# Optimization experiments

Measured on AMD Instinct MI355X. Metric: run time of the kernel, lower is better.

## Reference

```python
import jax, jax.numpy as jnp
import numpy as np

N_POINTS = 524288
N_VOXELS = 32768
C_IN = 6
GF = 64          # gf_dim
C_OUT = 256      # output_channels
HALF = C_OUT // 2


def _linear_params(key, fin, fout):
    kw, kb = jax.random.split(key)
    bound = 1.0 / np.sqrt(fin)
    W = jax.random.uniform(kw, (fin, fout), jnp.float32, -bound, bound)
    b = jax.random.uniform(kb, (fout,), jnp.float32, -bound, bound)
    return W, b


def setup_inputs() -> dict:
    key = jax.random.key(0)
    ks = jax.random.split(key, 8)
    inp_feat = jax.random.normal(ks[0], (N_POINTS, C_IN), dtype=jnp.float32)
    vox2point_idx = jax.random.randint(ks[1], (N_POINTS,), 0, N_VOXELS, dtype=jnp.int64)
    W1, b1 = _linear_params(ks[2], C_IN, GF)          # point_lin1
    W2, b2 = _linear_params(ks[3], GF, HALF)          # point_lin2
    Wv1, bv1 = _linear_params(ks[4], HALF, HALF)      # vox_lin1
    W3, b3 = _linear_params(ks[5], C_OUT, C_OUT)      # point_lin3
    W4, b4 = _linear_params(ks[6], C_OUT, C_OUT)      # point_lin4
    Wv2, bv2 = _linear_params(ks[7], C_OUT, C_OUT)    # vox_lin2
    return {
        "inp_feat": inp_feat, "vox2point_idx": vox2point_idx, "num_voxels": N_VOXELS,
        "W1": W1, "b1": b1, "W2": W2, "b2": b2, "Wv1": Wv1, "bv1": bv1,
        "W3": W3, "b3": b3, "W4": W4, "b4": b4, "Wv2": Wv2, "bv2": bv2,
    }


def reference(inp_feat, vox2point_idx, num_voxels,
              W1, b1, W2, b2, Wv1, bv1, W3, b3, W4, b4, Wv2, bv2):
    relu = jax.nn.relu
    # per-point MLP: [N,6] -> [N,64] -> [N,128]
    point_feat1 = relu(inp_feat @ W1 + b1)
    point_feat2 = relu(point_feat1 @ W2 + b2)
    # scatter-max pooling over voxels: [N,128] -> [V,128]
    occ_voxel_feat = jax.ops.segment_max(point_feat2, vox2point_idx,
                                         num_segments=num_voxels)
    occ_voxel_feat = relu(occ_voxel_feat @ Wv1 + bv1)
    # gather voxel feature back to points and concat: [N,128]+[N,128] -> [N,256]
    point_global_feat = occ_voxel_feat[vox2point_idx]
    point_feat3 = jnp.concatenate((point_global_feat, point_feat2), axis=-1)
    point_feat4 = relu(point_feat3 @ W3 + b3)
    point_feat5 = relu(point_feat4 @ W4 + b4)
    # second scatter-max pooling: [N,256] -> [V,256]
    occ_voxel_feat2 = jax.ops.segment_max(point_feat5, vox2point_idx,
                                          num_segments=num_voxels)
    occ_voxel_feat2 = relu(occ_voxel_feat2 @ Wv2 + bv2)
    return occ_voxel_feat2
```

## Files before the change

### kernel.cpp

```cpp
#include <hip/hip_runtime.h>


#define NPTS 524288
#define NVOX 32768

typedef _Float16 f16;
typedef _Float16 f16x8 __attribute__((ext_vector_type(8)));
typedef float f32x4 __attribute__((ext_vector_type(4)));

#define GLDS16(g, l)                                                          \
  __builtin_amdgcn_global_load_lds(                                           \
      (const __attribute__((address_space(1))) unsigned int*)(const void*)(g),\
      (__attribute__((address_space(3))) unsigned int*)(void*)(l), 16, 0, 0)

__global__ void k_fixidx(const int* __restrict__ raw, int* __restrict__ out) {
  bool is64 = true;
#pragma unroll
  for (int k = 0; k < 32; ++k)
    if (raw[2 * k + 1] != 0) is64 = false;
  int stride = gridDim.x * blockDim.x;
  for (int i = blockIdx.x * blockDim.x + threadIdx.x; i < NPTS; i += stride)
    out[i] = is64 ? raw[2 * i] : raw[i];
}

__global__ void k_hist(const int* __restrict__ idx, int* __restrict__ counts) {
  int stride = gridDim.x * blockDim.x;
  for (int i = blockIdx.x * blockDim.x + threadIdx.x; i < NPTS; i += stride)
    atomicAdd(&counts[idx[i]], 1);
}

__global__ void k_scan(const int* __restrict__ counts, int* __restrict__ offsets) {
  __shared__ int part[1024];
  __shared__ int sums[32];
  int t = threadIdx.x;
  int loc[32];
  int s = 0;
#pragma unroll
  for (int j = 0; j < 32; ++j) { loc[j] = counts[t * 32 + j]; s += loc[j]; }
  part[t] = s;
  __syncthreads();
  if (t < 32) {
    int run = 0;
    for (int j = 0; j < 32; ++j) { int tmp = part[t * 32 + j]; part[t * 32 + j] = run; run += tmp; }
    sums[t] = run;
  }
  __syncthreads();
  if (t == 0) {
    int run = 0;
    for (int i = 0; i < 32; ++i) { int tmp = sums[i]; sums[i] = run; run += tmp; }
  }
  __syncthreads();
  int b = part[t] + sums[t >> 5];
#pragma unroll
  for (int j = 0; j < 32; ++j) { offsets[t * 32 + j] = b; b += loc[j]; }
  if (t == 1023) offsets[NVOX] = b;
}

__global__ void k_scat(const int* __restrict__ idx, const int* __restrict__ offsets,
                       int* __restrict__ cursor, int* __restrict__ sp, int* __restrict__ sv) {
  int stride = gridDim.x * blockDim.x;
  for (int i = blockIdx.x * blockDim.x + threadIdx.x; i < NPTS; i += stride) {
    int v = idx[i];
    int pos = offsets[v] + atomicAdd(&cursor[v], 1);
    sp[pos] = i;
    sv[pos] = v;
  }
}

__global__ void k_wcast(const float* __restrict__ W, f16* __restrict__ Wt, int K, int N) {
  int g = blockIdx.x * blockDim.x + threadIdx.x;
  if (g >= K * N) return;
  int k = g / N, n = g % N;
  Wt[n * K + k] = (f16)W[g];
}

__global__ void k_castf(const float* __restrict__ in, f16* __restrict__ out, int n) {
  int stride = gridDim.x * blockDim.x;
  for (int i = blockIdx.x * blockDim.x + threadIdx.x; i < n; i += stride)
    out[i] = (f16)in[i];
}

template <int K, int N, int MODEA, bool SCATTER, bool OUTF32, bool WRITEO>
__global__ __launch_bounds__(256, 3) void k_gemm(
    const f16* __restrict__ A,
    const int* __restrict__ sv, const int* __restrict__ sp,
    const int* __restrict__ offs,
    const float* __restrict__ x, const float* __restrict__ W1, const float* __restrict__ b1,
    const f16* __restrict__ Bt,
    const float* __restrict__ bias,
    f16* __restrict__ Of16, float* __restrict__ Of32, int row0) {
  constexpr int NT = N / 128;
  __shared__ __align__(16) char smem[32768];
  __shared__ float xs[MODEA == 2 ? 768 : 1];
  __shared__ int svp[MODEA == 2 ? 128 : 1];
  __shared__ int svx[SCATTER ? 128 : 1];
  f16* As = (f16*)smem;
  f16* Bs = As + 128 * 64;

  int nwg = gridDim.x;
  int bid = blockIdx.x;
  int q = nwg >> 3;
  int swz = (bid & 7) * q + (bid >> 3);
  int tm = swz / NT, tn = swz % NT;
  int t = threadIdx.x;

  if (MODEA == 2) { if (t < 128) svp[t] = sp[row0 + tm * 128 + t]; }
  if (SCATTER) { if (t < 128) svx[t] = sv[row0 + tm * 128 + t]; }
  if (MODEA == 2) __syncthreads();

  int l = t & 63, w = t >> 6;
  int wm = w >> 1, wn = w & 1;
  int lrow = l & 15, lk = l >> 4;
  f32x4 acc[4][4] = {};

  constexpr int KT = K / 64;
#pragma unroll
  for (int kt = 0; kt < KT; ++kt) {
    int k0 = kt * 64;
#pragma unroll
    for (int i = 0; i < 4; ++i) {
      int n = i * 32 + (t >> 3);
      int clog = (t & 7) ^ (n & 7);
      GLDS16(Bt + (size_t)(tn * 128 + n) * K + k0 + clog * 8, Bs + i * 2048 + t * 8);
    }
    if constexpr (MODEA == 2) {
      for (int g = t; g < 768; g += 256) xs[g] = x[(size_t)svp[g / 6] * 6 + (g % 6)];
      __syncthreads();
      int j = t & 63;
      float wv[6];
#pragma unroll
      for (int i = 0; i < 6; ++i) wv[i] = W1[i * 64 + j];
      float bb = b1[j];
      int rb = (t >> 6) * 32;
#pragma unroll
      for (int rr = 0; rr < 32; ++rr) {
        int row = rb + rr;
        float a = bb;
#pragma unroll
        for (int i = 0; i < 6; ++i) a += xs[row * 6 + i] * wv[i];
        As[row * 64 + (((j >> 3) ^ (row & 7)) << 3) + (j & 7)] = (f16)fmaxf(a, 0.f);
      }
    } else {
#pragma unroll
      for (int i = 0; i < 4; ++i) {
        int row = i * 32 + (t >> 3);
        int clog = (t & 7) ^ (row & 7);
        GLDS16(A + (size_t)(tm * 128 + row) * K + k0 + clog * 8, As + i * 2048 + t * 8);
      }
    }
    __syncthreads();
#pragma unroll
    for (int ks = 0; ks < 2; ++ks) {
      f16x8 af[4], bf[4];
#pragma unroll
      for (int m = 0; m < 4; ++m) {
        int row = wm * 64 + m * 16 + lrow;
        int cp = (ks * 4 + lk) ^ (row & 7);
        af[m] = *(const f16x8*)(As + row * 64 + cp * 8);
      }
#pragma unroll
      for (int n = 0; n < 4; ++n) {
        int col = wn * 64 + n * 16 + lrow;
        int cp = (ks * 4 + lk) ^ (col & 7);
        bf[n] = *(const f16x8*)(Bs + col * 64 + cp * 8);
      }
#pragma unroll
      for (int m = 0; m < 4; ++m)
#pragma unroll
        for (int n = 0; n < 4; ++n)
          acc[m][n] = __builtin_amdgcn_mfma_f32_16x16x32_f16(af[m], bf[n], acc[m][n], 0, 0, 0);
    }
    __syncthreads();
  }

  if constexpr (WRITEO) {
#pragma unroll
    for (int m = 0; m < 4; ++m)
#pragma unroll
      for (int n = 0; n < 4; ++n)
#pragma unroll
        for (int j = 0; j < 4; ++j) {
          int row = wm * 64 + m * 16 + lk * 4 + j;
          int gc  = tn * 128 + wn * 64 + n * 16 + lrow;
          float val = fmaxf(acc[m][n][j] + bias[gc], 0.f);
          if constexpr (OUTF32) Of32[(size_t)(tm * 128 + row) * N + gc] = val;
          else                  Of16[(size_t)(tm * 128 + row) * N + gc] = (f16)val;
        }
  }

  if constexpr (SCATTER) {
    f16* tile = (f16*)smem;
#pragma unroll
    for (int m = 0; m < 4; ++m)
#pragma unroll
      for (int n = 0; n < 4; ++n)
#pragma unroll
        for (int j = 0; j < 4; ++j) {
          int row = wm * 64 + m * 16 + lk * 4 + j;
          int col = wn * 64 + n * 16 + lrow;
          tile[row * 128 + col] =
              (f16)fmaxf(acc[m][n][j] + bias[tn * 128 + col], 0.f);
        }
    __syncthreads();
    int c = t & 127, h = t >> 7;
    int r0l = h * 64;
    int gc = tn * 128 + c;
    int grow0 = row0 + tm * 128 + r0l;
    float run = 0.f;
    int curv = svx[r0l];
    for (int r = r0l; r < r0l + 64; ++r) {
      int v = svx[r];
      if (v != curv) {
        bool inter = (offs[curv] >= grow0) && (offs[curv + 1] <= grow0 + 64);
        if (inter) Of32[(size_t)curv * N + gc] = run;
        else atomicMax((int*)&Of32[(size_t)curv * N + gc], __float_as_int(run));
        curv = v; run = 0.f;
      }
      run = fmaxf(run, (float)tile[r * 128 + c]);
    }
    bool inter = (offs[curv] >= grow0) && (offs[curv + 1] <= grow0 + 64);
    if (inter) Of32[(size_t)curv * N + gc] = run;
    else atomicMax((int*)&Of32[(size_t)curv * N + gc], __float_as_int(run));
  }
}

__global__ __launch_bounds__(512, 2) void k_stage2(
    const f16* __restrict__ pf2, const f16* __restrict__ occ1,
    const int* __restrict__ sv, const int* __restrict__ offs,
    const f16* __restrict__ W3t, const float* __restrict__ b3,
    const f16* __restrict__ W4t, const float* __restrict__ b4,
    float* __restrict__ vox2f, int row0) {
  __shared__ __align__(16) char smem[8192 + 33792 + 33792];
  __shared__ int svx[64];
  f16* As  = (f16*)smem;
  f16* Bs  = (f16*)(smem + 8192);
  f16* pf5 = Bs;
  f16* pf4 = (f16*)(smem + 8192 + 33792);

  int nwg = gridDim.x;
  int bid = blockIdx.x;
  int q = nwg >> 3;
  int bm = (bid & 7) * q + (bid >> 3);
  int t = threadIdx.x;
  if (t < 64) svx[t] = sv[row0 + bm * 64 + t];
  __syncthreads();

  int l = t & 63, w = t >> 6;
  int lrow = l & 15, lk = l >> 4;

  {
    f32x4 acc[4][2] = {};
#pragma unroll
    for (int kt = 0; kt < 4; ++kt) {
      int k0 = kt * 64;
#pragma unroll
      for (int i = 0; i < 4; ++i) {
        int g = i * 512 + t;
        int n = g >> 3;
        int clog = (g & 7) ^ (n & 7);
        GLDS16(W3t + (size_t)n * 256 + k0 + clog * 8, Bs + g * 8);
      }
      {
        int r = t >> 3;
        int clog = (t & 7) ^ (r & 7);
        const f16* src;
        if (k0 < 128) src = occ1 + (size_t)svx[r] * 128 + k0 + clog * 8;
        else          src = pf2 + (size_t)(bm * 64 + r) * 128 + (k0 - 128) + clog * 8;
        GLDS16(src, As + t * 8);
      }
      __syncthreads();
#pragma unroll
      for (int ks = 0; ks < 2; ++ks) {
        f16x8 af[4], bf[2];
#pragma unroll
        for (int m = 0; m < 4; ++m) {
          int row = m * 16 + lrow;
          int cp = (ks * 4 + lk) ^ (row & 7);
          af[m] = *(const f16x8*)(As + row * 64 + cp * 8);
        }
#pragma unroll
        for (int n = 0; n < 2; ++n) {
          int col = w * 32 + n * 16 + lrow;
          int cp = (ks * 4 + lk) ^ (col & 7);
          bf[n] = *(const f16x8*)(Bs + col * 64 + cp * 8);
        }
#pragma unroll
        for (int m = 0; m < 4; ++m)
#pragma unroll
          for (int n = 0; n < 2; ++n)
            acc[m][n] = __builtin_amdgcn_mfma_f32_16x16x32_f16(af[m], bf[n], acc[m][n], 0, 0, 0);
      }
      __syncthreads();
    }
#pragma unroll
    for (int m = 0; m < 4; ++m)
#pragma unroll
      for (int n = 0; n < 2; ++n)
#pragma unroll
        for (int j = 0; j < 4; ++j) {
          int row  = m * 16 + lk * 4 + j;
          int colg = w * 32 + n * 16 + lrow;
          pf4[row * 264 + colg] = (f16)fmaxf(acc[m][n][j] + b3[colg], 0.f);
        }
  }
  __syncthreads();

  {
    f32x4 acc[4][2] = {};
#pragma unroll
    for (int kt = 0; kt < 4; ++kt) {
      int k0 = kt * 64;
#pragma unroll
      for (int i = 0; i < 4; ++i) {
        int g = i * 512 + t;
        int n = g >> 3;
        int clog = (g & 7) ^ (n & 7);
        GLDS16(W4t + (size_t)n * 256 + k0 + clog * 8, Bs + g * 8);
      }
      __syncthreads();
#pragma unroll
      for (int ks = 0; ks < 2; ++ks) {
        f16x8 af[4], bf[2];
#pragma unroll
        for (int m = 0; m < 4; ++m) {
          int row = m * 16 + lrow;
          int chunk = kt * 8 + ks * 4 + lk;
          af[m] = *(const f16x8*)(pf4 + row * 264 + chunk * 8);
        }
#pragma unroll
        for (int n = 0; n < 2; ++n) {
          int col = w * 32 + n * 16 + lrow;
          int cp = (ks * 4 + lk) ^ (col & 7);
          bf[n] = *(const f16x8*)(Bs + col * 64 + cp * 8);
        }
#pragma unroll
        for (int m = 0; m < 4; ++m)
#pragma unroll
          for (int n = 0; n < 2; ++n)
            acc[m][n] = __builtin_amdgcn_mfma_f32_16x16x32_f16(af[m], bf[n], acc[m][n], 0, 0, 0);
      }
      __syncthreads();
    }
#pragma unroll
    for (int m = 0; m < 4; ++m)
#pragma unroll
      for (int n = 0; n < 2; ++n)
#pragma unroll
        for (int j = 0; j < 4; ++j) {
          int row  = m * 16 + lk * 4 + j;
          int colg = w * 32 + n * 16 + lrow;
          pf5[row * 264 + colg] = (f16)fmaxf(acc[m][n][j] + b4[colg], 0.f);
        }
    __syncthreads();
    int c = t & 255, seg = t >> 8;
    int r0l = seg * 32;
    int grow0 = row0 + bm * 64 + r0l;
    float run = 0.f;
    int curv = svx[r0l];
    for (int r = r0l; r < r0l + 32; ++r) {
      int v = svx[r];
      if (v != curv) {
        bool inter = (offs[curv] >= grow0) && (offs[curv + 1] <= grow0 + 32);
        if (inter) vox2f[(size_t)curv * 256 + c] = run;
        else atomicMax((int*)&vox2f[(size_t)curv * 256 + c], __float_as_int(run));
        curv = v; run = 0.f;
      }
      run = fmaxf(run, (float)pf5[r * 264 + c]);
    }
    bool inter = (offs[curv] >= grow0) && (offs[curv + 1] <= grow0 + 32);
    if (inter) vox2f[(size_t)curv * 256 + c] = run;
    else atomicMax((int*)&vox2f[(size_t)curv * 256 + c], __float_as_int(run));
  }
}

extern "C" void kernel_launch(void* const* d_in, const int* in_sizes, int n_in,
                              void* d_out, int out_size, void* d_ws, size_t ws_size,
                              hipStream_t stream) {
  const float* x   = (const float*)d_in[0];
  const int*  idxr = (const int*)d_in[1];
  const float* W1  = (const float*)d_in[3];
  const float* b1  = (const float*)d_in[4];
  const float* W2  = (const float*)d_in[5];
  const float* b2  = (const float*)d_in[6];
  const float* Wv1 = (const float*)d_in[7];
  const float* bv1 = (const float*)d_in[8];
  const float* W3  = (const float*)d_in[9];
  const float* b3  = (const float*)d_in[10];
  const float* W4  = (const float*)d_in[11];
  const float* b4  = (const float*)d_in[12];
  const float* Wv2 = (const float*)d_in[13];
  const float* bv2 = (const float*)d_in[14];
  float* out = (float*)d_out;

  char* ws = (char*)d_ws;
  size_t off = 0;
  auto alloc = [&](size_t bytes) {
    void* p = ws + off;
    off = (off + bytes + 255) & ~(size_t)255;
    return p;
  };
  int* idx     = (int*)alloc((size_t)NPTS * 4);
  int* counts  = (int*)alloc((size_t)NVOX * 4);
  int* cursor  = (int*)alloc((size_t)NVOX * 4);
  int* offs    = (int*)alloc((size_t)(NVOX + 1) * 4);
  int* sp      = (int*)alloc((size_t)NPTS * 4);
  int* sv      = (int*)alloc((size_t)NPTS * 4);
  f16* W2t     = (f16*)alloc(64 * 128 * 2);
  f16* Wv1t    = (f16*)alloc(128 * 128 * 2);
  f16* W3t     = (f16*)alloc(256 * 256 * 2);
  f16* W4t     = (f16*)alloc(256 * 256 * 2);
  f16* Wv2t    = (f16*)alloc(256 * 256 * 2);
  float* vox1f = (float*)alloc((size_t)NVOX * 128 * 4);
  f16* vox1h   = (f16*)alloc((size_t)NVOX * 128 * 2);
  f16* occ1    = (f16*)alloc((size_t)NVOX * 128 * 2);
  float* vox2f = (float*)alloc((size_t)NVOX * 256 * 4);

  size_t rem = (ws_size > off) ? ws_size - off : 0;
  bool PF2FULL = rem >= (size_t)NPTS * 256 + 4096;
  int CH = 65536;
  f16* pf2   = (f16*)alloc(PF2FULL ? (size_t)NPTS * 256 : (size_t)CH * 256);
  f16* vox2h = pf2;

  hipMemsetAsync(counts, 0, (size_t)NVOX * 4, stream);
  hipMemsetAsync(cursor, 0, (size_t)NVOX * 4, stream);
  hipMemsetAsync(vox1f, 0, (size_t)NVOX * 128 * 4, stream);
  hipMemsetAsync(vox2f, 0, (size_t)NVOX * 256 * 4, stream);

  k_fixidx<<<2048, 256, 0, stream>>>(idxr, idx);
  k_wcast<<<(64 * 128 + 255) / 256, 256, 0, stream>>>(W2, W2t, 64, 128);
  k_wcast<<<(128 * 128 + 255) / 256, 256, 0, stream>>>(Wv1, Wv1t, 128, 128);
  k_wcast<<<(256 * 256 + 255) / 256, 256, 0, stream>>>(W3, W3t, 256, 256);
  k_wcast<<<(256 * 256 + 255) / 256, 256, 0, stream>>>(W4, W4t, 256, 256);
  k_wcast<<<(256 * 256 + 255) / 256, 256, 0, stream>>>(Wv2, Wv2t, 256, 256);
  k_hist<<<2048, 256, 0, stream>>>(idx, counts);
  k_scan<<<1, 1024, 0, stream>>>(counts, offs);
  k_scat<<<2048, 256, 0, stream>>>(idx, offs, cursor, sp, sv);

  if (PF2FULL)
    k_gemm<64, 128, 2, true, false, true><<<NPTS / 128, 256, 0, stream>>>(
        nullptr, sv, sp, offs, x, W1, b1, W2t, b2, pf2, vox1f, 0);
  else
    k_gemm<64, 128, 2, true, false, false><<<NPTS / 128, 256, 0, stream>>>(
        nullptr, sv, sp, offs, x, W1, b1, W2t, b2, nullptr, vox1f, 0);
  k_castf<<<2048, 256, 0, stream>>>(vox1f, vox1h, NVOX * 128);
  k_gemm<128, 128, 0, false, false, true><<<NVOX / 128, 256, 0, stream>>>(
      vox1h, nullptr, nullptr, nullptr, nullptr, nullptr, nullptr,
      Wv1t, bv1, occ1, nullptr, 0);

  if (PF2FULL) {
    k_stage2<<<NPTS / 64, 512, 0, stream>>>(
        pf2, occ1, sv, offs, W3t, b3, W4t, b4, vox2f, 0);
  } else {
    for (int c = 0; c < NPTS / CH; ++c) {
      int row0 = c * CH;
      k_gemm<64, 128, 2, false, false, true><<<CH / 128, 256, 0, stream>>>(
          nullptr, nullptr, sp, nullptr, x, W1, b1, W2t, b2, pf2, nullptr, row0);
      k_stage2<<<CH / 64, 512, 0, stream>>>(
          pf2, occ1, sv, offs, W3t, b3, W4t, b4, vox2f, row0);
    }
  }

  k_castf<<<2048, 256, 0, stream>>>(vox2f, vox2h, NVOX * 256);
  k_gemm<256, 256, 0, false, true, true><<<(NVOX / 128) * 2, 256, 0, stream>>>(
      vox2h, nullptr, nullptr, nullptr, nullptr, nullptr, nullptr,
      Wv2t, bv2, nullptr, out, 0);
}
```

Measured before the change: 416.8 us.

## Make stage2 persistent with register-resident weights and double-buffered A tiles

The fused W3/W4 point-MLP kernel becomes persistent: 1024 blocks each loop over several 64-row tiles. Each wave's slice of both weight matrices is loaded into registers once instead of being restaged through LDS for every tile. The next tile's gathered A operand (occ1 gather plus pf2) is prefetched into a second LDS buffer while the W4 GEMM runs. This cuts weight traffic and per-tile barriers, at the cost of heavy VGPR pressure from the 32 weight fragments, which may lower occupancy or cause spills.

Measured after the change: 466.5 us. +11.9%, slower.

```diff
diff --git a/kernel.cpp b/kernel.cpp
--- a/kernel.cpp
+++ b/kernel.cpp
@@ -229,147 +229,151 @@
     const int* __restrict__ sv, const int* __restrict__ offs,
     const f16* __restrict__ W3t, const float* __restrict__ b3,
     const f16* __restrict__ W4t, const float* __restrict__ b4,
-    float* __restrict__ vox2f, int row0) {
-  __shared__ __align__(16) char smem[8192 + 33792 + 33792];
+    float* __restrict__ vox2f, int row0, int tpb) {
+  __shared__ __align__(16) f16 AsBuf[2][64 * 256];
+  __shared__ __align__(16) f16 pf4[64 * 264];
   __shared__ int svx[64];
-  f16* As  = (f16*)smem;
-  f16* Bs  = (f16*)(smem + 8192);
-  f16* pf5 = Bs;
-  f16* pf4 = (f16*)(smem + 8192 + 33792);
+  f16* pf5 = pf4;
 
   int nwg = gridDim.x;
   int bid = blockIdx.x;
   int q = nwg >> 3;
   int bm = (bid & 7) * q + (bid >> 3);
   int t = threadIdx.x;
-  if (t < 64) svx[t] = sv[row0 + bm * 64 + t];
-  __syncthreads();
-
   int l = t & 63, w = t >> 6;
   int lrow = l & 15, lk = l >> 4;
 
-  {
-    f32x4 acc[4][2] = {};
-#pragma unroll
-    for (int kt = 0; kt < 4; ++kt) {
-      int k0 = kt * 64;
-#pragma unroll
-      for (int i = 0; i < 4; ++i) {
-        int g = i * 512 + t;
-        int n = g >> 3;
-        int clog = (g & 7) ^ (n & 7);
-        GLDS16(W3t + (size_t)n * 256 + k0 + clog * 8, Bs + g * 8);
-      }
-      {
-        int r = t >> 3;
-        int clog = (t & 7) ^ (r & 7);
-        const f16* src;
-        if (k0 < 128) src = occ1 + (size_t)svx[r] * 128 + k0 + clog * 8;
-        else          src = pf2 + (size_t)(bm * 64 + r) * 128 + (k0 - 128) + clog * 8;
-        GLDS16(src, As + t * 8);
-      }
+  f16x8 bf3[4][2][2], bf4[4][2][2];
+  float b3v[2], b4v[2];
+#pragma unroll
+  for (int n = 0; n < 2; ++n) {
+    int col = w * 32 + n * 16 + lrow;
+    b3v[n] = b3[col];
+    b4v[n] = b4[col];
+#pragma unroll
+    for (int kt = 0; kt < 4; ++kt)
+#pragma unroll
+      for (int ks = 0; ks < 2; ++ks) {
+        int koff = kt * 64 + (ks * 4 + lk) * 8;
+        bf3[kt][ks][n] = *(const f16x8*)(W3t + (size_t)col * 256 + koff);
+        bf4[kt][ks][n] = *(const f16x8*)(W4t + (size_t)col * 256 + koff);
+      }
+  }
+
+  auto STAGE = [&](int lt, f16* dst) {
+#pragma unroll
+    for (int ii = 0; ii < 4; ++ii) {
+      int g = ii * 512 + t;
+      int row = g >> 5, cs = g & 31;
+      int cl = cs ^ (row & 7);
+      const f16* src;
+      if (cl < 16) src = occ1 + (size_t)sv[row0 + lt * 64 + row] * 128 + cl * 8;
+      else         src = pf2 + (size_t)(lt * 64 + row) * 128 + (cl - 16) * 8;
+      GLDS16(src, dst + g * 8);
+    }
+  };
+
+  int t0 = bm * tpb;
+  int cur = 0;
+  STAGE(t0, AsBuf[0]);
+  __syncthreads();
+
+  for (int i = 0; i < tpb; ++i) {
+    int lt = t0 + i;
+    const f16* Acur = AsBuf[cur];
+
+    {
+      f32x4 acc[4][2] = {};
+#pragma unroll
+      for (int kt = 0; kt < 4; ++kt)
+#pragma unroll
+        for (int ks = 0; ks < 2; ++ks) {
+          f16x8 af[4];
+#pragma unroll
+          for (int m = 0; m < 4; ++m) {
+            int row = m * 16 + lrow;
+            int slot = kt * 8 + (((ks * 4 + lk)) ^ (row & 7));
+            af[m] = *(const f16x8*)(Acur + row * 256 + slot * 8);
+          }
+#pragma unroll
+          for (int m = 0; m < 4; ++m)
+#pragma unroll
+            for (int n = 0; n < 2; ++n)
+              acc[m][n] = __builtin_amdgcn_mfma_f32_16x16x32_f16(
+                  af[m], bf3[kt][ks][n], acc[m][n], 0, 0, 0);
+        }
+#pragma unroll
+      for (int m = 0; m < 4; ++m)
+#pragma unroll
+        for (int n = 0; n < 2; ++n)
+#pragma unroll
+          for (int j = 0; j < 4; ++j) {
+            int row  = m * 16 + lk * 4 + j;
+            int colg = w * 32 + n * 16 + lrow;
+            pf4[row * 264 + colg] = (f16)fmaxf(acc[m][n][j] + b3v[n], 0.f);
+          }
+    }
+    __syncthreads();
+
+    if (i + 1 < tpb) STAGE(lt + 1, AsBuf[cur ^ 1]);
+
+    {
+      f32x4 acc[4][2] = {};
+#pragma unroll
+      for (int kt = 0; kt < 4; ++kt)
+#pragma unroll
+        for (int ks = 0; ks < 2; ++ks) {
+          f16x8 af[4];
+#pragma unroll
+          for (int m = 0; m < 4; ++m) {
+            int row = m * 16 + lrow;
+            int chunk = kt * 8 + ks * 4 + lk;
+            af[m] = *(const f16x8*)(pf4 + row * 264 + chunk * 8);
+          }
+#pragma unroll
+          for (int m = 0; m < 4; ++m)
+#pragma unroll
+            for (int n = 0; n < 2; ++n)
+              acc[m][n] = __builtin_amdgcn_mfma_f32_16x16x32_f16(
+                  af[m], bf4[kt][ks][n], acc[m][n], 0, 0, 0);
+        }
       __syncthreads();
-#pragma unroll
-      for (int ks = 0; ks < 2; ++ks) {
-        f16x8 af[4], bf[2];
-#pragma unroll
-        for (int m = 0; m < 4; ++m) {
-          int row = m * 16 + lrow;
-          int cp = (ks * 4 + lk) ^ (row & 7);
-          af[m] = *(const f16x8*)(As + row * 64 + cp * 8);
+      if (t < 64) svx[t] = sv[row0 + lt * 64 + t];
+#pragma unroll
+      for (int m = 0; m < 4; ++m)
+#pragma unroll
+        for (int n = 0; n < 2; ++n)
+#pragma unroll
+          for (int j = 0; j < 4; ++j) {
+            int row  = m * 16 + lk * 4 + j;
+            int colg = w * 32 + n * 16 + lrow;
+            pf5[row * 264 + colg] = (f16)fmaxf(acc[m][n][j] + b4v[n], 0.f);
+          }
+    }
+    __syncthreads();
+
+    {
+      int c = t & 255, seg = t >> 8;
+      int r0l = seg * 32;
+      int grow0 = row0 + lt * 64 + r0l;
+      float run = 0.f;
+      int curv = svx[r0l];
+      for (int r = r0l; r < r0l + 32; ++r) {
+        int v = svx[r];
+        if (v != curv) {
+          bool inter = (offs[curv] >= grow0) && (offs[curv + 1] <= grow0 + 32);
+          if (inter) vox2f[(size_t)curv * 256 + c] = run;
+          else atomicMax((int*)&vox2f[(size_t)curv * 256 + c], __float_as_int(run));
+          curv = v; run = 0.f;
         }
-#pragma unroll
-        for (int n = 0; n < 2; ++n) {
-          int col = w * 32 + n * 16 + lrow;
-          int cp = (ks * 4 + lk) ^ (col & 7);
-          bf[n] = *(const f16x8*)(Bs + col * 64 + cp * 8);
-        }
-#pragma unroll
-        for (int m = 0; m < 4; ++m)
-#pragma unroll
-          for (int n = 0; n < 2; ++n)
-            acc[m][n] = __builtin_amdgcn_mfma_f32_16x16x32_f16(af[m], bf[n], acc[m][n], 0, 0, 0);
-      }
-      __syncthreads();
-    }
-#pragma unroll
-    for (int m = 0; m < 4; ++m)
-#pragma unroll
-      for (int n = 0; n < 2; ++n)
-#pragma unroll
-        for (int j = 0; j < 4; ++j) {
-          int row  = m * 16 + lk * 4 + j;
-          int colg = w * 32 + n * 16 + lrow;
-          pf4[row * 264 + colg] = (f16)fmaxf(acc[m][n][j] + b3[colg], 0.f);
-        }
-  }
-  __syncthreads();
-
-  {
-    f32x4 acc[4][2] = {};
-#pragma unroll
-    for (int kt = 0; kt < 4; ++kt) {
-      int k0 = kt * 64;
-#pragma unroll
-      for (int i = 0; i < 4; ++i) {
-        int g = i * 512 + t;
-        int n = g >> 3;
-        int clog = (g & 7) ^ (n & 7);
-        GLDS16(W4t + (size_t)n * 256 + k0 + clog * 8, Bs + g * 8);
-      }
-      __syncthreads();
-#pragma unroll
-      for (int ks = 0; ks < 2; ++ks) {
-        f16x8 af[4], bf[2];
-#pragma unroll
-        for (int m = 0; m < 4; ++m) {
-          int row = m * 16 + lrow;
-          int chunk = kt * 8 + ks * 4 + lk;
-          af[m] = *(const f16x8*)(pf4 + row * 264 + chunk * 8);
-        }
-#pragma unroll
-        for (int n = 0; n < 2; ++n) {
-          int col = w * 32 + n * 16 + lrow;
-          int cp = (ks * 4 + lk) ^ (col & 7);
-          bf[n] = *(const f16x8*)(Bs + col * 64 + cp * 8);
-        }
-#pragma unroll
-        for (int m = 0; m < 4; ++m)
-#pragma unroll
-          for (int n = 0; n < 2; ++n)
-            acc[m][n] = __builtin_amdgcn_mfma_f32_16x16x32_f16(af[m], bf[n], acc[m][n], 0, 0, 0);
-      }
-      __syncthreads();
-    }
-#pragma unroll
-    for (int m = 0; m < 4; ++m)
-#pragma unroll
-      for (int n = 0; n < 2; ++n)
-#pragma unroll
-        for (int j = 0; j < 4; ++j) {
-          int row  = m * 16 + lk * 4 + j;
-          int colg = w * 32 + n * 16 + lrow;
-          pf5[row * 264 + colg] = (f16)fmaxf(acc[m][n][j] + b4[colg], 0.f);
-        }
-    __syncthreads();
-    int c = t & 255, seg = t >> 8;
-    int r0l = seg * 32;
-    int grow0 = row0 + bm * 64 + r0l;
-    float run = 0.f;
-    int curv = svx[r0l];
-    for (int r = r0l; r < r0l + 32; ++r) {
-      int v = svx[r];
-      if (v != curv) {
-        bool inter = (offs[curv] >= grow0) && (offs[curv + 1] <= grow0 + 32);
-        if (inter) vox2f[(size_t)curv * 256 + c] = run;
-        else atomicMax((int*)&vox2f[(size_t)curv * 256 + c], __float_as_int(run));
-        curv = v; run = 0.f;
-      }
-      run = fmaxf(run, (float)pf5[r * 264 + c]);
-    }
-    bool inter = (offs[curv] >= grow0) && (offs[curv + 1] <= grow0 + 32);
-    if (inter) vox2f[(size_t)curv * 256 + c] = run;
-    else atomicMax((int*)&vox2f[(size_t)curv * 256 + c], __float_as_int(run));
+        run = fmaxf(run, (float)pf5[r * 264 + c]);
+      }
+      bool inter = (offs[curv] >= grow0) && (offs[curv + 1] <= grow0 + 32);
+      if (inter) vox2f[(size_t)curv * 256 + c] = run;
+      else atomicMax((int*)&vox2f[(size_t)curv * 256 + c], __float_as_int(run));
+    }
+    __syncthreads();
+    cur ^= 1;
   }
 }
 
@@ -448,15 +452,15 @@
       Wv1t, bv1, occ1, nullptr, 0);
 
   if (PF2FULL) {
-    k_stage2<<<NPTS / 64, 512, 0, stream>>>(
-        pf2, occ1, sv, offs, W3t, b3, W4t, b4, vox2f, 0);
+    k_stage2<<<1024, 512, 0, stream>>>(
+        pf2, occ1, sv, offs, W3t, b3, W4t, b4, vox2f, 0, (NPTS / 64) / 1024);
   } else {
     for (int c = 0; c < NPTS / CH; ++c) {
       int row0 = c * CH;
       k_gemm<64, 128, 2, false, false, true><<<CH / 128, 256, 0, stream>>>(
           nullptr, nullptr, sp, nullptr, x, W1, b1, W2t, b2, pf2, nullptr, row0);
-      k_stage2<<<CH / 64, 512, 0, stream>>>(
-          pf2, occ1, sv, offs, W3t, b3, W4t, b4, vox2f, row0);
+      k_stage2<<<1024, 512, 0, stream>>>(
+          pf2, occ1, sv, offs, W3t, b3, W4t, b4, vox2f, row0, (CH / 64) / 1024);
     }
   }
 
```

## Preload full A tile in stage2 and stream weights in K-slices of 32

Applied to the files above, without the earlier changes.

The stage2 kernel now loads the whole 64x256 A operand (gathered voxel features plus point features) into LDS once. It streams W3/W4 in 32-wide K slices through a smaller buffer and prefetches W4's first slice during the last W3 step. LDS use drops from about 75KB to about 50KB, which may let more workgroups fit per CU, at the cost of more barriers per K step. Separately, the first GEMM in the full-buffer path now writes pf2 as coalesced 16-byte stores from the LDS tile instead of scattered per-element stores.

New measurement: 401.8 us. 3.6% less time.

```diff
diff --git a/kernel.cpp b/kernel.cpp
--- a/kernel.cpp
+++ b/kernel.cpp
@@ -80,7 +80,7 @@
     out[i] = (f16)in[i];
 }
 
-template <int K, int N, int MODEA, bool SCATTER, bool OUTF32, bool WRITEO>
+template <int K, int N, int MODEA, bool SCATTER, bool OUTF32, bool WRITEO, bool WTILE>
 __global__ __launch_bounds__(256, 3) void k_gemm(
     const f16* __restrict__ A,
     const int* __restrict__ sv, const int* __restrict__ sp,
@@ -202,6 +202,14 @@
               (f16)fmaxf(acc[m][n][j] + bias[tn * 128 + col], 0.f);
         }
     __syncthreads();
+    if constexpr (WTILE) {
+      f16* dst = Of16 + (size_t)(row0 + tm * 128) * 128;
+#pragma unroll
+      for (int i = 0; i < 8; ++i) {
+        int g = i * 256 + t;
+        *(f16x8*)(dst + g * 8) = *(const f16x8*)(tile + g * 8);
+      }
+    }
     int c = t & 127, h = t >> 7;
     int r0l = h * 64;
     int gc = tn * 128 + c;
@@ -230,128 +238,143 @@
     const f16* __restrict__ W3t, const float* __restrict__ b3,
     const f16* __restrict__ W4t, const float* __restrict__ b4,
     float* __restrict__ vox2f, int row0) {
-  __shared__ __align__(16) char smem[8192 + 33792 + 33792];
+  __shared__ __align__(16) f16 Bs[256 * 32];
+  __shared__ __align__(16) f16 PF[64 * 264];
   __shared__ int svx[64];
-  f16* As  = (f16*)smem;
-  f16* Bs  = (f16*)(smem + 8192);
-  f16* pf5 = Bs;
-  f16* pf4 = (f16*)(smem + 8192 + 33792);
 
   int nwg = gridDim.x;
   int bid = blockIdx.x;
   int q = nwg >> 3;
   int bm = (bid & 7) * q + (bid >> 3);
   int t = threadIdx.x;
-  if (t < 64) svx[t] = sv[row0 + bm * 64 + t];
-  __syncthreads();
-
   int l = t & 63, w = t >> 6;
   int lrow = l & 15, lk = l >> 4;
 
+  if (t < 64) svx[t] = sv[row0 + bm * 64 + t];
+  __syncthreads();
+
+  f16* Afull = PF;
+#pragma unroll
+  for (int ii = 0; ii < 4; ++ii) {
+    int g = ii * 512 + t;
+    int row = g >> 5, cs = g & 31;
+    int cl = (cs & 24) | ((cs ^ row) & 7);
+    const f16* src;
+    if (cl < 16) src = occ1 + (size_t)svx[row] * 128 + cl * 8;
+    else         src = pf2 + (size_t)(bm * 64 + row) * 128 + (cl - 16) * 8;
+    GLDS16(src, Afull + g * 8);
+  }
+#pragma unroll
+  for (int ii = 0; ii < 2; ++ii) {
+    int g = ii * 512 + t;
+    int n = g >> 2, c = g & 3;
+    int cl = c ^ (n & 3);
+    GLDS16(W3t + (size_t)n * 256 + cl * 8, Bs + g * 8);
+  }
+  __syncthreads();
+
+  f32x4 acc[4][2] = {};
+
+#pragma unroll
+  for (int p = 0; p < 8; ++p) {
+    f16x8 af[4], bf[2];
+#pragma unroll
+    for (int m = 0; m < 4; ++m) {
+      int row = m * 16 + lrow;
+      int ab = p * 4 + lk;
+      int slot = (ab & 24) | ((ab ^ row) & 7);
+      af[m] = *(const f16x8*)(Afull + row * 256 + slot * 8);
+    }
+#pragma unroll
+    for (int n = 0; n < 2; ++n) {
+      int col = w * 32 + n * 16 + lrow;
+      int cp = lk ^ (col & 3);
+      bf[n] = *(const f16x8*)(Bs + col * 32 + cp * 8);
+    }
+#pragma unroll
+    for (int m = 0; m < 4; ++m)
+#pragma unroll
+      for (int n = 0; n < 2; ++n)
+        acc[m][n] = __builtin_amdgcn_mfma_f32_16x16x32_f16(af[m], bf[n], acc[m][n], 0, 0, 0);
+    __syncthreads();
+    const f16* Wsrc = (p < 7) ? W3t : W4t;
+    int kc = (p < 7) ? (p + 1) : 0;
+#pragma unroll
+    for (int ii = 0; ii < 2; ++ii) {
+      int g = ii * 512 + t;
+      int n = g >> 2, c = g & 3;
+      int cl = c ^ (n & 3);
+      GLDS16(Wsrc + (size_t)n * 256 + kc * 32 + cl * 8, Bs + g * 8);
+    }
+    __syncthreads();
+  }
+
+  f16* pf4 = PF;
+#pragma unroll
+  for (int m = 0; m < 4; ++m)
+#pragma unroll
+    for (int n = 0; n < 2; ++n)
+#pragma unroll
+      for (int j = 0; j < 4; ++j) {
+        int row  = m * 16 + lk * 4 + j;
+        int colg = w * 32 + n * 16 + lrow;
+        pf4[row * 264 + colg] = (f16)fmaxf(acc[m][n][j] + b3[colg], 0.f);
+      }
+  __syncthreads();
+
+#pragma unroll
+  for (int m = 0; m < 4; ++m)
+#pragma unroll
+    for (int n = 0; n < 2; ++n)
+      acc[m][n] = (f32x4){0.f, 0.f, 0.f, 0.f};
+
+#pragma unroll
+  for (int p = 0; p < 8; ++p) {
+    f16x8 af[4], bf[2];
+#pragma unroll
+    for (int m = 0; m < 4; ++m) {
+      int row = m * 16 + lrow;
+      int chunk = p * 4 + lk;
+      af[m] = *(const f16x8*)(pf4 + row * 264 + chunk * 8);
+    }
+#pragma unroll
+    for (int n = 0; n < 2; ++n) {
+      int col = w * 32 + n * 16 + lrow;
+      int cp = lk ^ (col & 3);
+      bf[n] = *(const f16x8*)(Bs + col * 32 + cp * 8);
+    }
+#pragma unroll
+    for (int m = 0; m < 4; ++m)
+#pragma unroll
+      for (int n = 0; n < 2; ++n)
+        acc[m][n] = __builtin_amdgcn_mfma_f32_16x16x32_f16(af[m], bf[n], acc[m][n], 0, 0, 0);
+    __syncthreads();
+    if (p < 7) {
+#pragma unroll
+      for (int ii = 0; ii < 2; ++ii) {
+        int g = ii * 512 + t;
+        int n = g >> 2, c = g & 3;
+        int cl = c ^ (n & 3);
+        GLDS16(W4t + (size_t)n * 256 + (p + 1) * 32 + cl * 8, Bs + g * 8);
+      }
+    }
+    __syncthreads();
+  }
+
+  f16* pf5 = PF;
+#pragma unroll
+  for (int m = 0; m < 4; ++m)
+#pragma unroll
+    for (int n = 0; n < 2; ++n)
+#pragma unroll
+      for (int j = 0; j < 4; ++j) {
+        int row  = m * 16 + lk * 4 + j;
+        int colg = w * 32 + n * 16 + lrow;
+        pf5[row * 264 + colg] = (f16)fmaxf(acc[m][n][j] + b4[colg], 0.f);
+      }
+  __syncthreads();
+
   {
-    f32x4 acc[4][2] = {};
-#pragma unroll
-    for (int kt = 0; kt < 4; ++kt) {
-      int k0 = kt * 64;
-#pragma unroll
-      for (int i = 0; i < 4; ++i) {
-        int g = i * 512 + t;
-        int n = g >> 3;
-        int clog = (g & 7) ^ (n & 7);
-        GLDS16(W3t + (size_t)n * 256 + k0 + clog * 8, Bs + g * 8);
-      }
-      {
-        int r = t >> 3;
-        int clog = (t & 7) ^ (r & 7);
-        const f16* src;
-        if (k0 < 128) src = occ1 + (size_t)svx[r] * 128 + k0 + clog * 8;
-        else          src = pf2 + (size_t)(bm * 64 + r) * 128 + (k0 - 128) + clog * 8;
-        GLDS16(src, As + t * 8);
-      }
-      __syncthreads();
-#pragma unroll
-      for (int ks = 0; ks < 2; ++ks) {
-        f16x8 af[4], bf[2];
-#pragma unroll
-        for (int m = 0; m < 4; ++m) {
-          int row = m * 16 + lrow;
-          int cp = (ks * 4 + lk) ^ (row & 7);
-          af[m] = *(const f16x8*)(As + row * 64 + cp * 8);
-        }
-#pragma unroll
-        for (int n = 0; n < 2; ++n) {
-          int col = w * 32 + n * 16 + lrow;
-          int cp = (ks * 4 + lk) ^ (col & 7);
-          bf[n] = *(const f16x8*)(Bs + col * 64 + cp * 8);
-        }
-#pragma unroll
-        for (int m = 0; m < 4; ++m)
-#pragma unroll
-          for (int n = 0; n < 2; ++n)
-            acc[m][n] = __builtin_amdgcn_mfma_f32_16x16x32_f16(af[m], bf[n], acc[m][n], 0, 0, 0);
-      }
-      __syncthreads();
-    }
-#pragma unroll
-    for (int m = 0; m < 4; ++m)
-#pragma unroll
-      for (int n = 0; n < 2; ++n)
-#pragma unroll
-        for (int j = 0; j < 4; ++j) {
-          int row  = m * 16 + lk * 4 + j;
-          int colg = w * 32 + n * 16 + lrow;
-          pf4[row * 264 + colg] = (f16)fmaxf(acc[m][n][j] + b3[colg], 0.f);
-        }
-  }
-  __syncthreads();
-
-  {
-    f32x4 acc[4][2] = {};
-#pragma unroll
-    for (int kt = 0; kt < 4; ++kt) {
-      int k0 = kt * 64;
-#pragma unroll
-      for (int i = 0; i < 4; ++i) {
-        int g = i * 512 + t;
-        int n = g >> 3;
-        int clog = (g & 7) ^ (n & 7);
-        GLDS16(W4t + (size_t)n * 256 + k0 + clog * 8, Bs + g * 8);
-      }
-      __syncthreads();
-#pragma unroll
-      for (int ks = 0; ks < 2; ++ks) {
-        f16x8 af[4], bf[2];
-#pragma unroll
-        for (int m = 0; m < 4; ++m) {
-          int row = m * 16 + lrow;
-          int chunk = kt * 8 + ks * 4 + lk;
-          af[m] = *(const f16x8*)(pf4 + row * 264 + chunk * 8);
-        }
-#pragma unroll
-        for (int n = 0; n < 2; ++n) {
-          int col = w * 32 + n * 16 + lrow;
-          int cp = (ks * 4 + lk) ^ (col & 7);
-          bf[n] = *(const f16x8*)(Bs + col * 64 + cp * 8);
-        }
-#pragma unroll
-        for (int m = 0; m < 4; ++m)
-#pragma unroll
-          for (int n = 0; n < 2; ++n)
-            acc[m][n] = __builtin_amdgcn_mfma_f32_16x16x32_f16(af[m], bf[n], acc[m][n], 0, 0, 0);
-      }
-      __syncthreads();
-    }
-#pragma unroll
-    for (int m = 0; m < 4; ++m)
-#pragma unroll
-      for (int n = 0; n < 2; ++n)
-#pragma unroll
-        for (int j = 0; j < 4; ++j) {
-          int row  = m * 16 + lk * 4 + j;
-          int colg = w * 32 + n * 16 + lrow;
-          pf5[row * 264 + colg] = (f16)fmaxf(acc[m][n][j] + b4[colg], 0.f);
-        }
-    __syncthreads();
     int c = t & 255, seg = t >> 8;
     int r0l = seg * 32;
     int grow0 = row0 + bm * 64 + r0l;
@@ -437,13 +460,13 @@
   k_scat<<<2048, 256, 0, stream>>>(idx, offs, cursor, sp, sv);
 
   if (PF2FULL)
-    k_gemm<64, 128, 2, true, false, true><<<NPTS / 128, 256, 0, stream>>>(
+    k_gemm<64, 128, 2, true, false, false, true><<<NPTS / 128, 256, 0, stream>>>(
         nullptr, sv, sp, offs, x, W1, b1, W2t, b2, pf2, vox1f, 0);
   else
-    k_gemm<64, 128, 2, true, false, false><<<NPTS / 128, 256, 0, stream>>>(
+    k_gemm<64, 128, 2, true, false, false, false><<<NPTS / 128, 256, 0, stream>>>(
         nullptr, sv, sp, offs, x, W1, b1, W2t, b2, nullptr, vox1f, 0);
   k_castf<<<2048, 256, 0, stream>>>(vox1f, vox1h, NVOX * 128);
-  k_gemm<128, 128, 0, false, false, true><<<NVOX / 128, 256, 0, stream>>>(
+  k_gemm<128, 128, 0, false, false, true, false><<<NVOX / 128, 256, 0, stream>>>(
       vox1h, nullptr, nullptr, nullptr, nullptr, nullptr, nullptr,
       Wv1t, bv1, occ1, nullptr, 0);
 
@@ -453,7 +476,7 @@
   } else {
     for (int c = 0; c < NPTS / CH; ++c) {
       int row0 = c * CH;
-      k_gemm<64, 128, 2, false, false, true><<<CH / 128, 256, 0, stream>>>(
+      k_gemm<64, 128, 2, false, false, true, false><<<CH / 128, 256, 0, stream>>>(
           nullptr, nullptr, sp, nullptr, x, W1, b1, W2t, b2, pf2, nullptr, row0);
       k_stage2<<<CH / 64, 512, 0, stream>>>(
           pf2, occ1, sv, offs, W3t, b3, W4t, b4, vox2f, row0);
@@ -461,7 +484,7 @@
   }
 
   k_castf<<<2048, 256, 0, stream>>>(vox2f, vox2h, NVOX * 256);
-  k_gemm<256, 256, 0, false, true, true><<<(NVOX / 128) * 2, 256, 0, stream>>>(
+  k_gemm<256, 256, 0, false, true, true, false><<<(NVOX / 128) * 2, 256, 0, stream>>>(
       vox2h, nullptr, nullptr, nullptr, nullptr, nullptr, nullptr,
       Wv2t, bv2, nullptr, out, 0);
 }
```
